# Performance work log

Measured on AMD Instinct MI355X. Metric: run time of the kernel, lower is better.

The kernel has to match this reference:

```python
import jax, jax.numpy as jnp
import numpy as np

B, C, H, W = 16384, 1, 2048, 1
HID = 5


def setup_inputs() -> dict:
    key = jax.random.key(0)
    kx, kl, k1, k2, k3, k4 = jax.random.split(key, 6)
    x = jax.random.normal(kx, (B, C, H, W), dtype=jnp.float32)
    # random ragged lengths in [1, H]; zero out padded tail so the module's
    # (x != 0).any(dim=2) mask recovers exactly these lengths
    lengths = jax.random.randint(kl, (B,), 1, H + 1)
    t_idx = jnp.arange(H)
    valid = (t_idx[None, :] < lengths[:, None])  # [B, H]
    x = x * valid[:, None, :, None].astype(jnp.float32)
    s = 1.0 / np.sqrt(HID)
    W_ih = jax.random.uniform(k1, (4 * HID, 1), minval=-s, maxval=s, dtype=jnp.float32)
    W_hh = jax.random.uniform(k2, (4 * HID, HID), minval=-s, maxval=s, dtype=jnp.float32)
    b_ih = jax.random.uniform(k3, (4 * HID,), minval=-s, maxval=s, dtype=jnp.float32)
    b_hh = jax.random.uniform(k4, (4 * HID,), minval=-s, maxval=s, dtype=jnp.float32)
    return {"x": x, "W_ih": W_ih, "W_hh": W_hh, "b_ih": b_ih, "b_hh": b_hh}


def reference(x, W_ih, W_hh, b_ih, b_hh):
    b, c, h, w = x.shape
    feats = c * w  # == 1 (LSTM input_size)
    xr = x.reshape(b, h, feats)  # [B, T, 1]
    mask = jnp.any(xr != 0, axis=2)  # [B, T]
    lengths = mask.sum(axis=1).astype(jnp.int32)  # [B]

    bias = b_ih + b_hh  # [4H]
    # precompute input projection for all timesteps: [B, T, 4H]
    x_proj = jnp.einsum('btf,gf->btg', xr, W_ih) + bias
    xs = jnp.moveaxis(x_proj, 1, 0)  # [T, B, 4H]

    h0 = jnp.zeros((b, HID), dtype=x.dtype)
    c0 = jnp.zeros((b, HID), dtype=x.dtype)

    def step(carry, inp):
        hp, cp = carry
        xg, t = inp
        gates = xg + hp @ W_hh.T  # [B, 4H]
        i, f, g, o = jnp.split(gates, 4, axis=1)
        i = jax.nn.sigmoid(i)
        f = jax.nn.sigmoid(f)
        g = jnp.tanh(g)
        o = jax.nn.sigmoid(o)
        cn = f * cp + i * g
        hn = o * jnp.tanh(cn)
        # packed semantics: only advance state while t < length (per sample)
        upd = (t < lengths)[:, None]
        hn = jnp.where(upd, hn, hp)
        cn = jnp.where(upd, cn, cp)
        return (hn, cn), None

    (hT, cT), _ = jax.lax.scan(step, (h0, c0), (xs, jnp.arange(h)))
    return hT[None]  # [1, B, HID] matching torch h shape
```

## Files before the change

### kernel.cpp

```cpp
#include <hip/hip_runtime.h>

#define Bn    16384
#define Tn    2048
#define HIDn  5
#define NBINS 2048

typedef float v2f __attribute__((ext_vector_type(2)));

static __device__ __forceinline__ float rcp_fast(float v) {
    return __builtin_amdgcn_rcpf(v);
}
static __device__ __forceinline__ float med3(float x, float lo, float hi) {
    return __builtin_amdgcn_fmed3f(x, lo, hi);
}

template <int K>
static __device__ __forceinline__ float bcast8(float v) {
    return __int_as_float(
        __builtin_amdgcn_ds_swizzle(__float_as_int(v), (K << 5) | 0x18));
}

__global__ void zero_kernel(int* __restrict__ gbins) {
    gbins[blockIdx.x * 256 + threadIdx.x] = 0;
}

__global__ __launch_bounds__(256) void len_kernel(const float* __restrict__ x,
                                                  int* __restrict__ lengths,
                                                  int* __restrict__ gbins) {
    const int gtid = blockIdx.x * 256 + threadIdx.x;
    const int row  = gtid >> 6;
    const int lane = threadIdx.x & 63;
    const float4* r = reinterpret_cast<const float4*>(x + (size_t)row * Tn);
    int cnt = 0;
    #pragma unroll
    for (int i = 0; i < Tn / 4 / 64; ++i) {
        float4 v = r[i * 64 + lane];
        cnt += (v.x != 0.0f) + (v.y != 0.0f) + (v.z != 0.0f) + (v.w != 0.0f);
    }
    #pragma unroll
    for (int off = 32; off > 0; off >>= 1) cnt += __shfl_xor(cnt, off, 64);
    if (lane == 0) {
        lengths[row] = cnt;
        const int d = max(0, min(NBINS - 1, NBINS - cnt));
        atomicAdd(&gbins[d], 1);
    }
}

__global__ __launch_bounds__(1024) void sort_kernel(const int* __restrict__ lengths,
                                                    const int* __restrict__ gbins,
                                                    int* __restrict__ perm) {
    __shared__ int bins[NBINS];
    __shared__ int bsum[1024];
    const int tid = threadIdx.x;
    bins[tid]        = gbins[tid];
    bins[tid + 1024] = gbins[tid + 1024];
    __syncthreads();
    const int a0 = bins[2 * tid], a1 = bins[2 * tid + 1];
    const int s = a0 + a1;
    bsum[tid] = s;
    __syncthreads();
    int acc = s;
    for (int off = 1; off < 1024; off <<= 1) {
        int v = (tid >= off) ? bsum[tid - off] : 0;
        __syncthreads();
        acc += v;
        bsum[tid] = acc;
        __syncthreads();
    }
    const int excl = acc - s;
    bins[2 * tid]     = excl;
    bins[2 * tid + 1] = excl + a0;
    __syncthreads();
    for (int i = tid; i < Bn; i += 1024) {
        int d = NBINS - lengths[i];
        d = max(0, min(NBINS - 1, d));
        const int p = atomicAdd(&bins[d], 1);
        perm[p] = i;
    }
}

__global__ __launch_bounds__(256, 2) void lstm_kernel(const float* __restrict__ x,
                                                      const float* __restrict__ Wih,
                                                      const float* __restrict__ Whh,
                                                      const float* __restrict__ bih,
                                                      const float* __restrict__ bhh,
                                                      const int* __restrict__ lengths,
                                                      const int* __restrict__ perm,
                                                      float* __restrict__ out) {
    const int gtid = blockIdx.x * 256 + threadIdx.x;
    const int grp  = gtid >> 3;
    const int lsub = threadIdx.x & 7;
    const int k    = min(lsub, 4);

    const int b   = perm[grp];
    const int len = lengths[b];

    v2f wihA, wihB, bA, bB, whhA[HIDn], whhB[HIDn];
    {
        const int gi = k, gf = 5 + k, gg = 10 + k, go = 15 + k;
        wihA = (v2f){ Wih[gi] * 0.5f, Wih[gf] * 0.5f };
        wihB = (v2f){ Wih[gg],        Wih[go] * 0.5f };
        bA   = (v2f){ (bih[gi] + bhh[gi]) * 0.5f, (bih[gf] + bhh[gf]) * 0.5f };
        bB   = (v2f){ (bih[gg] + bhh[gg]),        (bih[go] + bhh[go]) * 0.5f };
        #pragma unroll
        for (int kk = 0; kk < HIDn; ++kk) {
            whhA[kk] = (v2f){ Whh[gi * HIDn + kk] * 0.5f, Whh[gf * HIDn + kk] * 0.5f };
            whhB[kk] = (v2f){ Whh[gg * HIDn + kk],        Whh[go * HIDn + kk] * 0.5f };
        }
    }

    const float* xrow = x + (size_t)b * Tn;
    float h0 = 0, h1 = 0, h2 = 0, h3 = 0, h4 = 0;
    float hq = 0, c = 0;

    float4 xq = *reinterpret_cast<const float4*>(xrow);
    for (int t = 0; __any(t < len); t += 4) {
        const float4 xn = *reinterpret_cast<const float4*>(xrow + min(t + 4, Tn - 4));
        const float xs[4] = { xq.x, xq.y, xq.z, xq.w };
        #pragma unroll
        for (int s = 0; s < 4; ++s) {
            const float xv = xs[s];
            const v2f xA = xv * wihA + bA;
            const v2f xB = xv * wihB + bB;
            const v2f tA0 = h0 * whhA[0] + xA;
            const v2f tB0 = h0 * whhB[0] + xB;
            const v2f mA2 = h2 * whhA[2];
            const v2f mB2 = h2 * whhB[2];
            const v2f tA1 = h1 * whhA[1] + mA2;
            const v2f tB1 = h1 * whhB[1] + mB2;
            const v2f mA4 = h4 * whhA[4];
            const v2f mB4 = h4 * whhB[4];
            const v2f tA2 = h3 * whhA[3] + mA4;
            const v2f tB2 = h3 * whhB[3] + mB4;
            const v2f pA = (tA0 + tA1) + tA2;
            const v2f pB = (tB0 + tB1) + tB2;
            v2f tA, tB;
            tA.x = med3(pA.x, -4.0f, 4.0f);  tA.y = med3(pA.y, -4.0f, 4.0f);
            tB.x = med3(pB.x, -4.0f, 4.0f);  tB.y = med3(pB.y, -4.0f, 4.0f);
            const v2f zA = tA * tA, zB = tB * tB;
            const v2f nA = (zA * 21.0f + 1260.0f) * zA + 10395.0f;
            const v2f nB = (zB * 21.0f + 1260.0f) * zB + 10395.0f;
            const v2f dA = ((zA + 210.0f) * zA + 4725.0f) * zA + 10395.0f;
            const v2f dB = ((zB + 210.0f) * zB + 4725.0f) * zB + 10395.0f;
            const float rIx = rcp_fast(dA.x);
            const float rIy = rcp_fast(dA.y);
            const float rGx = rcp_fast(dB.x);
            const float rGy = rcp_fast(dB.y);
            const v2f pnA = tA * nA, pnB = tB * nB;
            const float ti = pnA.x * rIx;
            const float tf = pnA.y * rIy;
            const float tg = pnB.x * rGx;
            const float to = pnB.y * rGy;

            const float qf = fmaf(tf, c, c);
            const float qi = fmaf(ti, tg, tg);
            const float cn = fmaf(qf, 0.5f, 0.5f * qi);
            const float oo = fmaf(to, 0.5f, 0.5f);

            const float tc = med3(cn, -4.0f, 4.0f);
            const float zc = tc * tc;
            const float nc = fmaf(zc, fmaf(zc, 21.0f, 1260.0f), 10395.0f);
            const float dc = fmaf(zc, fmaf(zc, zc + 210.0f, 4725.0f), 10395.0f);
            const float rc  = rcp_fast(dc);
            const float pre = (tc * nc) * oo;
            const float hn  = pre * rc;

            const bool upd = (t + s) < len;
            c  = upd ? cn : c;
            hq = upd ? hn : hq;

            h0 = bcast8<0>(hq);
            h1 = bcast8<1>(hq);
            h2 = bcast8<2>(hq);
            h3 = bcast8<3>(hq);
            h4 = bcast8<4>(hq);
        }
        xq = xn;
    }

    if (lsub < HIDn) out[(size_t)b * HIDn + lsub] = hq;
}

extern "C" void kernel_launch(void* const* d_in, const int* in_sizes, int n_in,
                              void* d_out, int out_size, void* d_ws, size_t ws_size,
                              hipStream_t stream) {
    const float* x   = (const float*)d_in[0];
    const float* Wih = (const float*)d_in[1];
    const float* Whh = (const float*)d_in[2];
    const float* bih = (const float*)d_in[3];
    const float* bhh = (const float*)d_in[4];
    float* out = (float*)d_out;

    int* lengths = (int*)d_ws;
    int* perm    = lengths + Bn;
    int* gbins   = perm + Bn;

    zero_kernel<<<NBINS / 256, 256, 0, stream>>>(gbins);
    len_kernel<<<Bn / 4, 256, 0, stream>>>(x, lengths, gbins);
    sort_kernel<<<1, 1024, 0, stream>>>(lengths, gbins, perm);
    lstm_kernel<<<Bn * 8 / 256, 256, 0, stream>>>(x, Wih, Whh, bih, bhh,
                                                  lengths, perm, out);
}
```

Measured before the change: 588.6 us.

## Replace Pade tanh with rcp-free Chebyshev polynomial activations and wave priority

Replaces the rational Padé tanh approximations for the i, f and g gates and the cell tanh with host-fitted polynomial approximations in z=w^2, evaluated by Estrin's scheme. This drops four of the five reciprocals per step and rescales the weights so the clamp range becomes [-1,1]. The output gate now uses exp2 plus a reciprocal, and the cell state is stored scaled. It also raises wave priority for alternate groups of 256 blocks. The trade-off is extra FMAs per step and a possible accuracy change from the polynomial degree and the clamping.

Result: slower. 759.8 us (+29.1%).

```diff
diff --git a/kernel.cpp b/kernel.cpp
--- a/kernel.cpp
+++ b/kernel.cpp
@@ -1,4 +1,5 @@
 #include <hip/hip_runtime.h>
+#include <cmath>
 
 #define Bn    16384
 #define Tn    2048
@@ -10,6 +11,9 @@
 static __device__ __forceinline__ float rcp_fast(float v) {
     return __builtin_amdgcn_rcpf(v);
 }
+static __device__ __forceinline__ float exp2_fast(float v) {
+    return __builtin_amdgcn_exp2f(v);
+}
 static __device__ __forceinline__ float med3(float x, float lo, float hi) {
     return __builtin_amdgcn_fmed3f(x, lo, hi);
 }
@@ -18,6 +22,44 @@
 static __device__ __forceinline__ float bcast8(float v) {
     return __int_as_float(
         __builtin_amdgcn_ds_swizzle(__float_as_int(v), (K << 5) | 0x18));
+}
+
+struct ActCoeffs {
+    float sig[14];
+    float gg[10];
+    float spine[14];
+};
+
+template <int N>
+static __device__ __forceinline__ float poly_eval(const float* C, float z) {
+    const float z2 = z * z, z4 = z2 * z2, z8 = z4 * z4;
+    if constexpr (N == 14) {
+        const float A0 = fmaf(z, C[1],  C[0]),  A1 = fmaf(z, C[3],  C[2]);
+        const float A2 = fmaf(z, C[5],  C[4]),  A3 = fmaf(z, C[7],  C[6]);
+        const float A4 = fmaf(z, C[9],  C[8]),  A5 = fmaf(z, C[11], C[10]);
+        const float A6 = fmaf(z, C[13], C[12]);
+        const float B0 = fmaf(z2, A1, A0), B1 = fmaf(z2, A3, A2), B2 = fmaf(z2, A5, A4);
+        const float D0 = fmaf(z4, B1, B0), D1 = fmaf(z4, A6, B2);
+        return fmaf(z8, D1, D0);
+    } else {
+        const float A0 = fmaf(z, C[1], C[0]),  A1 = fmaf(z, C[3], C[2]);
+        const float A2 = fmaf(z, C[5], C[4]),  A3 = fmaf(z, C[7], C[6]);
+        const float A4 = fmaf(z, C[9], C[8]);
+        const float B0 = fmaf(z2, A1, A0), B1 = fmaf(z2, A3, A2);
+        const float D0 = fmaf(z4, B1, B0);
+        return fmaf(z8, A4, D0);
+    }
+}
+
+static __device__ __forceinline__ v2f poly_eval2_14(const float* C, v2f z) {
+    const v2f z2 = z * z, z4 = z2 * z2, z8 = z4 * z4;
+    const v2f A0 = z * C[1]  + C[0],  A1 = z * C[3]  + C[2];
+    const v2f A2 = z * C[5]  + C[4],  A3 = z * C[7]  + C[6];
+    const v2f A4 = z * C[9]  + C[8],  A5 = z * C[11] + C[10];
+    const v2f A6 = z * C[13] + C[12];
+    const v2f B0 = z2 * A1 + A0, B1 = z2 * A3 + A2, B2 = z2 * A5 + A4;
+    const v2f D0 = z4 * B1 + B0, D1 = z4 * A6 + B2;
+    return z8 * D1 + D0;
 }
 
 __global__ void zero_kernel(int* __restrict__ gbins) {
@@ -86,32 +128,38 @@
                                                       const float* __restrict__ bhh,
                                                       const int* __restrict__ lengths,
                                                       const int* __restrict__ perm,
-                                                      float* __restrict__ out) {
+                                                      float* __restrict__ out,
+                                                      ActCoeffs AC) {
     const int gtid = blockIdx.x * 256 + threadIdx.x;
     const int grp  = gtid >> 3;
     const int lsub = threadIdx.x & 7;
     const int k    = min(lsub, 4);
 
+    if ((blockIdx.x >> 8) & 1) __builtin_amdgcn_s_setprio(1);
+
     const int b   = perm[grp];
     const int len = lengths[b];
 
+    const float SA = 0.125f;
+    const float SG = 0.25f;
+    const float SO = -1.4426950408889634f;
     v2f wihA, wihB, bA, bB, whhA[HIDn], whhB[HIDn];
     {
         const int gi = k, gf = 5 + k, gg = 10 + k, go = 15 + k;
-        wihA = (v2f){ Wih[gi] * 0.5f, Wih[gf] * 0.5f };
-        wihB = (v2f){ Wih[gg],        Wih[go] * 0.5f };
-        bA   = (v2f){ (bih[gi] + bhh[gi]) * 0.5f, (bih[gf] + bhh[gf]) * 0.5f };
-        bB   = (v2f){ (bih[gg] + bhh[gg]),        (bih[go] + bhh[go]) * 0.5f };
+        wihA = (v2f){ Wih[gi] * SA, Wih[gf] * SA };
+        wihB = (v2f){ Wih[gg] * SG, Wih[go] * SO };
+        bA   = (v2f){ (bih[gi] + bhh[gi]) * SA, (bih[gf] + bhh[gf]) * SA };
+        bB   = (v2f){ (bih[gg] + bhh[gg]) * SG, (bih[go] + bhh[go]) * SO };
         #pragma unroll
         for (int kk = 0; kk < HIDn; ++kk) {
-            whhA[kk] = (v2f){ Whh[gi * HIDn + kk] * 0.5f, Whh[gf * HIDn + kk] * 0.5f };
-            whhB[kk] = (v2f){ Whh[gg * HIDn + kk],        Whh[go * HIDn + kk] * 0.5f };
+            whhA[kk] = (v2f){ Whh[gi * HIDn + kk] * SA, Whh[gf * HIDn + kk] * SA };
+            whhB[kk] = (v2f){ Whh[gg * HIDn + kk] * SG, Whh[go * HIDn + kk] * SO };
         }
     }
 
     const float* xrow = x + (size_t)b * Tn;
     float h0 = 0, h1 = 0, h2 = 0, h3 = 0, h4 = 0;
-    float hq = 0, c = 0;
+    float hq = 0, c4 = 0;
 
     float4 xq = *reinterpret_cast<const float4*>(xrow);
     for (int t = 0; __any(t < len); t += 4) {
@@ -134,39 +182,30 @@
             const v2f tB2 = h3 * whhB[3] + mB4;
             const v2f pA = (tA0 + tA1) + tA2;
             const v2f pB = (tB0 + tB1) + tB2;
-            v2f tA, tB;
-            tA.x = med3(pA.x, -4.0f, 4.0f);  tA.y = med3(pA.y, -4.0f, 4.0f);
-            tB.x = med3(pB.x, -4.0f, 4.0f);  tB.y = med3(pB.y, -4.0f, 4.0f);
-            const v2f zA = tA * tA, zB = tB * tB;
-            const v2f nA = (zA * 21.0f + 1260.0f) * zA + 10395.0f;
-            const v2f nB = (zB * 21.0f + 1260.0f) * zB + 10395.0f;
-            const v2f dA = ((zA + 210.0f) * zA + 4725.0f) * zA + 10395.0f;
-            const v2f dB = ((zB + 210.0f) * zB + 4725.0f) * zB + 10395.0f;
-            const float rIx = rcp_fast(dA.x);
-            const float rIy = rcp_fast(dA.y);
-            const float rGx = rcp_fast(dB.x);
-            const float rGy = rcp_fast(dB.y);
-            const v2f pnA = tA * nA, pnB = tB * nB;
-            const float ti = pnA.x * rIx;
-            const float tf = pnA.y * rIy;
-            const float tg = pnB.x * rGx;
-            const float to = pnB.y * rGy;
-
-            const float qf = fmaf(tf, c, c);
-            const float qi = fmaf(ti, tg, tg);
-            const float cn = fmaf(qf, 0.5f, 0.5f * qi);
-            const float oo = fmaf(to, 0.5f, 0.5f);
-
-            const float tc = med3(cn, -4.0f, 4.0f);
-            const float zc = tc * tc;
-            const float nc = fmaf(zc, fmaf(zc, 21.0f, 1260.0f), 10395.0f);
-            const float dc = fmaf(zc, fmaf(zc, zc + 210.0f, 4725.0f), 10395.0f);
-            const float rc  = rcp_fast(dc);
-            const float pre = (tc * nc) * oo;
-            const float hn  = pre * rc;
+
+            v2f wA;
+            wA.x = med3(pA.x, -1.0f, 1.0f);
+            wA.y = med3(pA.y, -1.0f, 1.0f);
+            const v2f zA = wA * wA;
+            const v2f Ps = poly_eval2_14(AC.sig, zA);
+            const v2f sAB = wA * Ps + 0.5f;
+
+            const float wg  = med3(pB.x, -1.0f, 1.0f);
+            const float Pg  = poly_eval<10>(AC.gg, wg * wg);
+            const float tg4 = wg * Pg;
+
+            const float eO = exp2_fast(pB.y);
+            const float oo = rcp_fast(1.0f + eO);
+
+            const float cn4 = fmaf(sAB.y, c4, sAB.x * tg4);
+
+            const float cc = med3(cn4, -1.0f, 1.0f);
+            const float Pc = poly_eval<14>(AC.spine, cc * cc);
+            const float ts = cc * Pc;
+            const float hn = ts * oo;
 
             const bool upd = (t + s) < len;
-            c  = upd ? cn : c;
+            c4 = upd ? cn4 : c4;
             hq = upd ? hn : hq;
 
             h0 = bcast8<0>(hq);
@@ -179,6 +218,31 @@
     }
 
     if (lsub < HIDn) out[(size_t)b * HIDn + lsub] = hq;
+}
+
+static void tanh_base_poly(int N, double* c) {
+    double yj[16], fj[16];
+    for (int j = 0; j < N; ++j) {
+        const double v = cos(M_PI * (2 * j + 1) / (2.0 * N));
+        const double y = 0.5 + 0.5 * v;
+        const double xx = 4.0 * sqrt(y);
+        yj[j] = y;
+        fj[j] = tanh(xx) / xx;
+    }
+    for (int k = 1; k < N; ++k)
+        for (int j = N - 1; j >= k; --j)
+            fj[j] = (fj[j] - fj[j - 1]) / (yj[j] - yj[j - k]);
+    for (int i = 0; i < 16; ++i) c[i] = 0.0;
+    c[0] = fj[N - 1];
+    int deg = 0;
+    for (int j = N - 2; j >= 0; --j) {
+        for (int i = deg; i >= 0; --i) {
+            c[i + 1] += c[i];
+            c[i] = -yj[j] * c[i];
+        }
+        ++deg;
+        c[0] += fj[j];
+    }
 }
 
 extern "C" void kernel_launch(void* const* d_in, const int* in_sizes, int n_in,
@@ -195,9 +259,21 @@
     int* perm    = lengths + Bn;
     int* gbins   = perm + Bn;
 
+    ActCoeffs AC;
+    {
+        double c14[16], c10[16];
+        tanh_base_poly(14, c14);
+        tanh_base_poly(10, c10);
+        for (int i = 0; i < 14; ++i) {
+            AC.sig[i]   = (float)(2.0 * c14[i]);
+            AC.spine[i] = (float)(4.0 * c14[i]);
+        }
+        for (int i = 0; i < 10; ++i) AC.gg[i] = (float)c10[i];
+    }
+
     zero_kernel<<<NBINS / 256, 256, 0, stream>>>(gbins);
     len_kernel<<<Bn / 4, 256, 0, stream>>>(x, lengths, gbins);
     sort_kernel<<<1, 1024, 0, stream>>>(lengths, gbins, perm);
     lstm_kernel<<<Bn * 8 / 256, 256, 0, stream>>>(x, Wih, Whh, bih, bhh,
-                                                  lengths, perm, out);
-}
+                                                  lengths, perm, out, AC);
+}
```
